# Kernel tuning notes

Hardware: AMD Instinct MI355X
Metric: run time of the kernel (lower is better)

The kernel has to match this reference:

```python
import jax, jax.numpy as jnp
import numpy as np

MODES = (16, 16)
EMBED_DIM = 64
NUM_HEADS = 8


def spectral_conv(x, w):
    """FNO-style spectral conv. x: [B,S,Ci,H,W]; w: [Ci,Co,mx,my,2] (real/imag)."""
    wc = w[..., 0] + 1j * w[..., 1]
    H, W = x.shape[-2], x.shape[-1]
    mx, my = wc.shape[2], wc.shape[3]
    xf = jnp.fft.rfft2(x)                                   # [B,S,Ci,H,W//2+1]
    of = jnp.einsum('bsixy,ioxy->bsoxy', xf[..., :mx, :my], wc)
    out_f = jnp.zeros(x.shape[:2] + (wc.shape[1], H, W // 2 + 1), dtype=of.dtype)
    out_f = out_f.at[..., :mx, :my].set(of)
    return jnp.fft.irfft2(out_f, s=(H, W))


def log_cpb_bias(n_sub_x, n_sub_y, w1, b1, w2):
    """Swin-v2-style log-spaced continuous position bias -> [heads, S, S]."""
    cx = jnp.arange(n_sub_x, dtype=jnp.float32)
    cy = jnp.arange(n_sub_y, dtype=jnp.float32)
    coords = jnp.stack(jnp.meshgrid(cx, cy, indexing='ij'), axis=-1).reshape(-1, 2)
    rel = coords[:, None, :] - coords[None, :, :]           # [S,S,2]
    rel = jnp.sign(rel) * jnp.log1p(jnp.abs(rel))
    h = jax.nn.relu(rel @ w1 + b1)                          # [S,S,hidden]
    bias = h @ w2                                           # [S,S,heads]
    return jnp.transpose(bias, (2, 0, 1))


def _unflatten(f, num_heads, embed_dim):
    # [B,S,h*d,H,W] -> [B,h,S,d,H,W]
    B, S = f.shape[0], f.shape[1]
    f = f.reshape(B, S, num_heads, embed_dim, f.shape[-2], f.shape[-1])
    return jnp.transpose(f, (0, 2, 1, 3, 4, 5))


def setup_inputs() -> dict:
    key = jax.random.key(0)
    ks = jax.random.split(key, 9)
    B, S, D, H, W = 2, 64, EMBED_DIM, 32, 32
    hd = NUM_HEADS * D
    mx, my = MODES
    scale = 0.02
    return {
        'seq': jax.random.normal(ks[0], (B, S, D, H, W), dtype=jnp.float32),
        'wq': scale * jax.random.normal(ks[1], (D, hd, mx, my, 2), dtype=jnp.float32),
        'wk': scale * jax.random.normal(ks[2], (D, hd, mx, my, 2), dtype=jnp.float32),
        'wv': scale * jax.random.normal(ks[3], (D, hd, mx, my, 2), dtype=jnp.float32),
        'wo': scale * jax.random.normal(ks[4], (hd, D, mx, my, 2), dtype=jnp.float32),
        'cpb_w1': scale * jax.random.normal(ks[5], (2, D), dtype=jnp.float32),
        'cpb_b1': jnp.zeros((D,), dtype=jnp.float32),
        'cpb_w2': scale * jax.random.normal(ks[6], (D, NUM_HEADS), dtype=jnp.float32),
        'n_sub_x': 8,
        'n_sub_y': 8,
    }


def reference(seq, wq, wk, wv, wo, cpb_w1, cpb_b1, cpb_w2, n_sub_x, n_sub_y):
    q = _unflatten(spectral_conv(seq, wq), NUM_HEADS, EMBED_DIM)  # [B,h,S,d,H,W]
    k = _unflatten(spectral_conv(seq, wk), NUM_HEADS, EMBED_DIM)
    v = _unflatten(spectral_conv(seq, wv), NUM_HEADS, EMBED_DIM)

    bias = log_cpb_bias(n_sub_x, n_sub_y, cpb_w1, cpb_b1, cpb_w2)  # [h,S,S]

    d, H, W = q.shape[-3], q.shape[-2], q.shape[-1]
    scale = 1.0 / jnp.sqrt(jnp.asarray(d * H * W, dtype=q.dtype))
    scores = jnp.einsum('bhqdxy,bhkdxy->bhqk', q, k) * scale + bias[None]
    attn = jax.nn.softmax(scores, axis=-1)
    sa = jnp.einsum('bhqk,bhkdxy->bhqdxy', attn, v)          # [B,h,S,d,H,W]

    # _flatten: [B,h,S,d,H,W] -> [B,S,h*d,H,W]
    sa = jnp.transpose(sa, (0, 2, 1, 3, 4, 5))
    B, S = sa.shape[0], sa.shape[1]
    sa = sa.reshape(B, S, NUM_HEADS * EMBED_DIM, H, W)
    return spectral_conv(sa, wo)
```

## Files before the change

### kernel.cpp

```cpp
#include <hip/hip_runtime.h>

#define TWO_PI 6.28318530717958647692f

#define NH 8
#define CH 128
#define NCH 2

#define OFF_XM   0ull
#define OFF_WTA  (OFF_XM + 8388608ull)
#define OFF_WTB  (OFF_WTA + 16777216ull)
#define OFF_PO   (OFF_WTB + 16777216ull)
#define OFF_ATTN (OFF_PO + 16777216ull)
#define WS_TOTAL (OFF_ATTN + 262144ull)

typedef short bf16x8 __attribute__((ext_vector_type(8)));
typedef float f32x4 __attribute__((ext_vector_type(4)));
#define MFMA_B16(a, b, c) __builtin_amdgcn_mfma_f32_16x16x32_bf16(a, b, c, 0, 0, 0)

__device__ __forceinline__ float bl(unsigned u) { return __uint_as_float(u << 16); }
__device__ __forceinline__ unsigned short f2b(float f) {
    unsigned u = __float_as_uint(f);
    return (unsigned short)((u + 0x7fffu + ((u >> 16) & 1u)) >> 16);
}
__device__ __forceinline__ unsigned pack2(float lo, float hi) {
    return (unsigned)f2b(lo) | ((unsigned)f2b(hi) << 16);
}

__device__ __forceinline__ bf16x8 mkfrag(const unsigned* __restrict__ Wt, int co_l, int ri,
                                         int ci0, bool dc) {
    unsigned a0 = Wt[(ci0 + 0) * 64 + (co_l ^ (ci0 + 0))];
    unsigned a1 = Wt[(ci0 + 1) * 64 + (co_l ^ (ci0 + 1))];
    unsigned a2 = Wt[(ci0 + 2) * 64 + (co_l ^ (ci0 + 2))];
    unsigned a3 = Wt[(ci0 + 3) * 64 + (co_l ^ (ci0 + 3))];
    uint4 r;
    if (ri) {
        if (dc) { r.x = 0u; r.y = 0u; r.z = 0u; r.w = 0u; }
        else {
            r.x = (a0 >> 16) | (a0 << 16); r.y = (a1 >> 16) | (a1 << 16);
            r.z = (a2 >> 16) | (a2 << 16); r.w = (a3 >> 16) | (a3 << 16);
        }
    } else {
        r.x = a0 ^ 0x80000000u; r.y = a1 ^ 0x80000000u;
        r.z = a2 ^ 0x80000000u; r.w = a3 ^ 0x80000000u;
    }
    return __builtin_bit_cast(bf16x8, r);
}

__global__ __launch_bounds__(256) void k_transpose2(const float* __restrict__ srcA, unsigned* __restrict__ dstA, int kindA,
                                                    const float* __restrict__ srcB, unsigned* __restrict__ dstB, int kindB,
                                                    int m0) {
    const float* in = (blockIdx.z == 0) ? srcA : srcB;
    unsigned* outp = (blockIdx.z == 0) ? dstA : dstB;
    int kind = (blockIdx.z == 0) ? kindA : kindB;
    __shared__ unsigned T[16][65];
    int tid = threadIdx.x;
    int r0 = blockIdx.x * 64;
    int ci, h;
    if (kind == 2) { h = r0 >> 12; ci = (r0 >> 6) & 63; }
    else           { ci = r0 >> 9; h = (r0 >> 6) & 7; }
    int ml0 = blockIdx.y * 16;
    int u = (m0 + ml0) >> 4;
    const float2* in2 = (const float2*)in;
    #pragma unroll
    for (int p = 0; p < 4; ++p) {
        int f = tid + p * 256;
        int row = f >> 4, mc = f & 15;
        float fac = (kind == 0) ? (mc > 0 ? 1.41421356f : (u > 0 ? 0.70710678f : 1.f))
                  : (kind == 1) ? (mc > 0 ? 1.f : (u > 0 ? 0.5f : 1.f)) : 1.f;
        float2 v = in2[(size_t)(r0 + row) * 256 + m0 + ml0 + mc];
        T[mc][row] = pack2(v.x * fac, v.y * fac);
    }
    __syncthreads();
    #pragma unroll
    for (int p = 0; p < 4; ++p) {
        int f = tid + p * 256;
        int ml = f >> 6, co = f & 63;
        outp[((size_t)((ml0 + ml) * 8 + h) << 12) + ci * 64 + co] = T[ml][co];
    }
}

__global__ __launch_bounds__(256) void k_rfft_y(const float* __restrict__ seq,
                                                float2* __restrict__ T) {
    __shared__ float c32[32], s32[32];
    __shared__ float fld[32][33];
    int tid = threadIdx.x;
    int bc = blockIdx.x;
    if (tid < 32) { float s, c; __sincosf(TWO_PI * tid / 32.0f, &s, &c); c32[tid] = c; s32[tid] = s; }
    float4 v = ((const float4*)(seq + (size_t)bc * 1024))[tid];
    int x = tid >> 3, y4 = (tid & 7) * 4;
    fld[x][y4] = v.x; fld[x][y4 + 1] = v.y; fld[x][y4 + 2] = v.z; fld[x][y4 + 3] = v.w;
    __syncthreads();
    float2* op = T + (size_t)bc * 512;
    #pragma unroll
    for (int p = 0; p < 2; ++p) {
        int e = tid + p * 256;
        int xx = e >> 4, vv = e & 15;
        float sr = 0.f, si = 0.f;
        #pragma unroll
        for (int y = 0; y < 32; ++y) {
            float f = fld[xx][y];
            int ph = (vv * y) & 31;
            sr = fmaf(f, c32[ph], sr);
            si = fmaf(-f, s32[ph], si);
        }
        float2 t; t.x = sr; t.y = si;
        op[e] = t;
    }
}

__global__ __launch_bounds__(256) void k_rfft_x(const float2* __restrict__ T,
                                                unsigned short* __restrict__ XM) {
    __shared__ float c32[32], s32[32];
    __shared__ float2 t[8][512];
    int tid = threadIdx.x;
    int cig = blockIdx.x;
    int bs = blockIdx.y;
    if (tid < 32) { float s, c; __sincosf(TWO_PI * tid / 32.0f, &s, &c); c32[tid] = c; s32[tid] = s; }
    const float4* src = (const float4*)(T + ((size_t)bs * 64 + cig * 8) * 512);
    #pragma unroll
    for (int p = 0; p < 8; ++p) {
        int idx = tid + p * 256;
        float4 w = src[idx];
        int ch = idx >> 8, r2 = idx & 255;
        float2 t0; t0.x = w.x; t0.y = w.y;
        float2 t1; t1.x = w.z; t1.y = w.w;
        t[ch][r2 * 2] = t0; t[ch][r2 * 2 + 1] = t1;
    }
    __syncthreads();
    int u = tid >> 4, vv = tid & 15;
    unsigned outw[8];
    for (int ch = 0; ch < 8; ++ch) {
        float xr = 0.f, xi = 0.f;
        #pragma unroll
        for (int x = 0; x < 32; ++x) {
            float2 tv = t[ch][x * 16 + vv];
            int ph = (u * x) & 31;
            float c = c32[ph], s = s32[ph];
            xr += tv.x * c + tv.y * s;
            xi += tv.y * c - tv.x * s;
        }
        outw[ch] = pack2(xr, xi);
    }
    uint4* op = (uint4*)(XM + (((size_t)tid * 128 + bs) * 64 + cig * 8) * 2);
    uint4 a, b;
    a.x = outw[0]; a.y = outw[1]; a.z = outw[2]; a.w = outw[3];
    b.x = outw[4]; b.y = outw[5]; b.z = outw[6]; b.w = outw[7];
    op[0] = a; op[1] = b;
}

__global__ __launch_bounds__(512) void k_qks(const unsigned short* __restrict__ XM,
                                             const unsigned* __restrict__ WQ,
                                             const unsigned* __restrict__ WK,
                                             float* __restrict__ part, int mbase) {
    __shared__ __align__(16) unsigned char Xs[16384];
    __shared__ __align__(16) unsigned Wq[4096];
    __shared__ __align__(16) unsigned Wk[4096];
    __shared__ __align__(16) unsigned char Qs[16384];
    __shared__ __align__(16) unsigned char Ks[16384];
    int tid = threadIdx.x;
    int mg = blockIdx.x, h = blockIdx.y, b = blockIdx.z;
    int lane = tid & 63, w = tid >> 6;
    int lr = lane & 15, lg = lane >> 4;
    int wr = w & 1, wc = w >> 1;
    int sxa = (lr & 7) << 4;
    int ri = lr & 1;
    f32x4 zf = {0.f, 0.f, 0.f, 0.f};
    f32x4 sacc[2];
    sacc[0] = zf; sacc[1] = zf;
    for (int mm = 0; mm < 4; ++mm) {
        int ml = mg * 4 + mm;
        int mode = mbase + ml;
        bool dc = (mode == 0);
        __syncthreads();
        {
            const unsigned short* xg = XM + ((size_t)mode * 128 + b * 64) * 128;
            #pragma unroll
            for (int p = 0; p < 2; ++p) {
                int g = tid + p * 512; int row = g >> 4, c16 = g & 15;
                uint4 v = *(const uint4*)(xg + row * 128 + c16 * 8);
                *(uint4*)(Xs + row * 256 + ((c16 * 16) ^ ((row & 7) << 4))) = v;
            }
        }
        {
            const unsigned* tq = WQ + ((size_t)(ml * 8 + h) << 12);
            const unsigned* tk = WK + ((size_t)(ml * 8 + h) << 12);
            #pragma unroll
            for (int p = 0; p < 16; ++p) {
                int idx = tid + p * 512;
                int r = idx & 4095;
                int ci = r >> 6, co = r & 63;
                if (idx < 4096) Wq[ci * 64 + (co ^ ci)] = tq[r];
                else            Wk[ci * 64 + (co ^ ci)] = tk[r];
            }
        }
        __syncthreads();
        {
            f32x4 qa[2][2], ka[2][2];
            #pragma unroll
            for (int m = 0; m < 2; ++m)
                #pragma unroll
                for (int n = 0; n < 2; ++n) { qa[m][n] = zf; ka[m][n] = zf; }
            #pragma unroll
            for (int ks = 0; ks < 4; ++ks) {
                int kb = (ks * 64 + lg * 16) ^ sxa;
                int ci0 = ks * 16 + lg * 4;
                bf16x8 a0 = *(const bf16x8*)(Xs + (wr * 32 + lr) * 256 + kb);
                bf16x8 a1 = *(const bf16x8*)(Xs + (wr * 32 + 16 + lr) * 256 + kb);
                #pragma unroll
                for (int n = 0; n < 2; ++n) {
                    int co_l = wc * 16 + n * 8 + (lr >> 1);
                    bf16x8 bq = mkfrag(Wq, co_l, ri, ci0, dc);
                    bf16x8 bk = mkfrag(Wk, co_l, ri, ci0, dc);
                    qa[0][n] = MFMA_B16(a0, bq, qa[0][n]);
                    qa[1][n] = MFMA_B16(a1, bq, qa[1][n]);
                    ka[0][n] = MFMA_B16(a0, bk, ka[0][n]);
                    ka[1][n] = MFMA_B16(a1, bk, ka[1][n]);
                }
            }
            #pragma unroll
            for (int m = 0; m < 2; ++m)
                #pragma unroll
                for (int n = 0; n < 2; ++n) {
                    int colb = (wc * 32 + n * 16 + lr) * 2;
                    #pragma unroll
                    for (int r = 0; r < 4; ++r) {
                        int row = wr * 32 + m * 16 + lg * 4 + r;
                        int swz = (row & 7) << 4;
                        *(unsigned short*)(Qs + row * 256 + (colb ^ swz)) = f2b(qa[m][n][r]);
                        *(unsigned short*)(Ks + row * 256 + (colb ^ swz)) = f2b(ka[m][n][r]);
                    }
                }
        }
        __syncthreads();
        {
            #pragma unroll
            for (int ks = 0; ks < 4; ++ks) {
                int kb = (ks * 64 + lg * 16) ^ sxa;
                bf16x8 a0 = *(const bf16x8*)(Qs + (wr * 32 + lr) * 256 + kb);
                bf16x8 a1 = *(const bf16x8*)(Qs + (wr * 32 + 16 + lr) * 256 + kb);
                bf16x8 b0 = *(const bf16x8*)(Ks + (wc * 16 + lr) * 256 + kb);
                sacc[0] = MFMA_B16(a0, b0, sacc[0]);
                sacc[1] = MFMA_B16(a1, b0, sacc[1]);
            }
        }
    }
    float* pp = part + (((size_t)((mbase >> 2) + mg) * 16 + b * 8 + h) << 12);
    #pragma unroll
    for (int m = 0; m < 2; ++m)
        #pragma unroll
        for (int r = 0; r < 4; ++r)
            pp[(wr * 32 + m * 16 + lg * 4 + r) * 64 + wc * 16 + lr] = sacc[m][r];
}

__global__ void k_softmax(const float* __restrict__ part,
                          const float* __restrict__ w1, const float* __restrict__ b1,
                          const float* __restrict__ w2, unsigned short* __restrict__ attnb) {
    int j = threadIdx.x;
    int i = blockIdx.x;
    int bh = blockIdx.y;
    int h = bh & 7;
    float s = 0.f;
    for (int mg = 0; mg < 64; ++mg)
        s += part[(((size_t)mg * 16 + bh) * 64 + i) * 64 + j];
    float dx = (float)((i >> 3) - (j >> 3));
    float dy = (float)((i & 7) - (j & 7));
    float rx = (dx > 0.f ? 1.f : (dx < 0.f ? -1.f : 0.f)) * log1pf(fabsf(dx));
    float ry = (dy > 0.f ? 1.f : (dy < 0.f ? -1.f : 0.f)) * log1pf(fabsf(dy));
    float bias = 0.f;
    for (int l = 0; l < 64; ++l) {
        float hv = fmaxf(rx * w1[l] + ry * w1[64 + l] + b1[l], 0.f);
        bias = fmaf(hv, w2[l * NH + h], bias);
    }
    s = s * (1.0f / 262144.0f) + bias;
    float m = s;
    for (int o = 32; o >= 1; o >>= 1) m = fmaxf(m, __shfl_xor(m, o));
    float e = expf(s - m);
    float t = e;
    for (int o = 32; o >= 1; o >>= 1) t += __shfl_xor(t, o);
    attnb[((size_t)bh * 64 + i) * 64 + j] = f2b(e / t);
}

__global__ __launch_bounds__(512) void k_savo(const unsigned short* __restrict__ XM,
                                              const unsigned* __restrict__ WV,
                                              const unsigned* __restrict__ WO,
                                              const unsigned short* __restrict__ attnb,
                                              float* __restrict__ outf, int mbase) {
    __shared__ __align__(16) unsigned char Xs[16384];
    __shared__ __align__(16) unsigned Wv[4096];
    __shared__ __align__(16) unsigned Wo[4096];
    __shared__ __align__(16) unsigned char Vt[16384];
    __shared__ __align__(16) unsigned char Ss[16384];
    int tid = threadIdx.x;
    int ml = blockIdx.x, b = blockIdx.y;
    int mode = mbase + ml;
    bool dc = (mode == 0);
    int lane = tid & 63, w = tid >> 6;
    int lr = lane & 15, lg = lane >> 4;
    int wr = w & 1, wc = w >> 1;
    int sxa = (lr & 7) << 4;
    int ri = lr & 1;
    f32x4 zf = {0.f, 0.f, 0.f, 0.f};
    {
        const unsigned short* xg = XM + ((size_t)mode * 128 + b * 64) * 128;
        #pragma unroll
        for (int p = 0; p < 2; ++p) {
            int g = tid + p * 512; int row = g >> 4, c16 = g & 15;
            uint4 v = *(const uint4*)(xg + row * 128 + c16 * 8);
            *(uint4*)(Xs + row * 256 + ((c16 * 16) ^ ((row & 7) << 4))) = v;
        }
    }
    f32x4 oacc[2][2];
    oacc[0][0] = zf; oacc[0][1] = zf; oacc[1][0] = zf; oacc[1][1] = zf;
    for (int h = 0; h < NH; ++h) {
        __syncthreads();
        {
            const unsigned* tv = WV + ((size_t)(ml * 8 + h) << 12);
            const unsigned* to = WO + ((size_t)(ml * 8 + h) << 12);
            #pragma unroll
            for (int p = 0; p < 16; ++p) {
                int idx = tid + p * 512;
                int r = idx & 4095;
                int ci = r >> 6, co = r & 63;
                if (idx < 4096) Wv[ci * 64 + (co ^ ci)] = tv[r];
                else            Wo[ci * 64 + (co ^ ci)] = to[r];
            }
        }
        bf16x8 af[2][2];
        #pragma unroll
        for (int m = 0; m < 2; ++m)
            #pragma unroll
            for (int ks = 0; ks < 2; ++ks) {
                int irow = wr * 32 + m * 16 + lr;
                af[m][ks] = *(const bf16x8*)(attnb + (((size_t)(b * 8 + h) * 64 + irow) * 64 + ks * 32 + lg * 8));
            }
        __syncthreads();
        {
            f32x4 va[2][2];
            va[0][0] = zf; va[0][1] = zf; va[1][0] = zf; va[1][1] = zf;
            #pragma unroll
            for (int ks = 0; ks < 4; ++ks) {
                int kb = (ks * 64 + lg * 16) ^ sxa;
                int ci0 = ks * 16 + lg * 4;
                bf16x8 a0 = *(const bf16x8*)(Xs + (wr * 32 + lr) * 256 + kb);
                bf16x8 a1 = *(const bf16x8*)(Xs + (wr * 32 + 16 + lr) * 256 + kb);
                #pragma unroll
                for (int n = 0; n < 2; ++n) {
                    int co_l = wc * 16 + n * 8 + (lr >> 1);
                    bf16x8 bb = mkfrag(Wv, co_l, ri, ci0, dc);
                    va[0][n] = MFMA_B16(a0, bb, va[0][n]);
                    va[1][n] = MFMA_B16(a1, bb, va[1][n]);
                }
            }
            #pragma unroll
            for (int m = 0; m < 2; ++m)
                #pragma unroll
                for (int n = 0; n < 2; ++n) {
                    int cp = wc * 32 + n * 16 + lr;
                    int j0 = wr * 32 + m * 16 + lg * 4;
                    uint2 t;
                    t.x = pack2(va[m][n][0], va[m][n][1]);
                    t.y = pack2(va[m][n][2], va[m][n][3]);
                    *(uint2*)(Vt + cp * 128 + ((j0 * 2) ^ ((cp & 7) << 4))) = t;
                }
        }
        __syncthreads();
        {
            f32x4 sa_[2][2];
            sa_[0][0] = zf; sa_[0][1] = zf; sa_[1][0] = zf; sa_[1][1] = zf;
            #pragma unroll
            for (int ks = 0; ks < 2; ++ks) {
                #pragma unroll
                for (int n = 0; n < 2; ++n) {
                    int cp = wc * 32 + n * 16 + lr;
                    bf16x8 bb = *(const bf16x8*)(Vt + cp * 128 + ((ks * 64 + lg * 16) ^ ((cp & 7) << 4)));
                    sa_[0][n] = MFMA_B16(af[0][ks], bb, sa_[0][n]);
                    sa_[1][n] = MFMA_B16(af[1][ks], bb, sa_[1][n]);
                }
            }
            #pragma unroll
            for (int m = 0; m < 2; ++m)
                #pragma unroll
                for (int n = 0; n < 2; ++n) {
                    int colb = (wc * 32 + n * 16 + lr) * 2;
                    #pragma unroll
                    for (int r = 0; r < 4; ++r) {
                        int row = wr * 32 + m * 16 + lg * 4 + r;
                        *(unsigned short*)(Ss + row * 256 + (colb ^ ((row & 7) << 4))) = f2b(sa_[m][n][r]);
                    }
                }
        }
        __syncthreads();
        {
            #pragma unroll
            for (int ks = 0; ks < 4; ++ks) {
                int kb = (ks * 64 + lg * 16) ^ sxa;
                int ci0 = ks * 16 + lg * 4;
                bf16x8 a0 = *(const bf16x8*)(Ss + (wr * 32 + lr) * 256 + kb);
                bf16x8 a1 = *(const bf16x8*)(Ss + (wr * 32 + 16 + lr) * 256 + kb);
                #pragma unroll
                for (int n = 0; n < 2; ++n) {
                    int co_l = wc * 16 + n * 8 + (lr >> 1);
                    bf16x8 bb = mkfrag(Wo, co_l, ri, ci0, false);
                    oacc[0][n] = MFMA_B16(a0, bb, oacc[0][n]);
                    oacc[1][n] = MFMA_B16(a1, bb, oacc[1][n]);
                }
            }
        }
    }
    #pragma unroll
    for (int m = 0; m < 2; ++m)
        #pragma unroll
        for (int n = 0; n < 2; ++n)
            #pragma unroll
            for (int r = 0; r < 4; ++r) {
                int i = wr * 32 + m * 16 + lg * 4 + r;
                int c2p = wc * 32 + n * 16 + lr;
                outf[((size_t)mode * 128 + b * 64 + i) * 128 + c2p] = oacc[m][n][r];
            }
}

__global__ __launch_bounds__(256) void k_irfft_v(const float* __restrict__ outf,
                                                 float2* __restrict__ G) {
    __shared__ float c32[32], s32[32];
    __shared__ float2 mf[256][8];
    int tid = threadIdx.x;
    int cg = blockIdx.x;
    int bs = blockIdx.y;
    if (tid < 32) { float s, c; __sincosf(TWO_PI * tid / 32.0f, &s, &c); c32[tid] = c; s32[tid] = s; }
    #pragma unroll
    for (int p = 0; p < 4; ++p) {
        int idx = tid + p * 256;
        int mode = idx >> 2, q = idx & 3;
        float4 v = *(const float4*)(outf + ((size_t)mode * 128 + bs) * 128 + cg * 16 + q * 4);
        float2 t0; t0.x = v.x; t0.y = v.y;
        float2 t1; t1.x = v.z; t1.y = v.w;
        mf[mode][q * 2] = t0; mf[mode][q * 2 + 1] = t1;
    }
    __syncthreads();
    #pragma unroll 1
    for (int p = 0; p < 2; ++p) {
        int e = tid + p * 256;
        int u = e >> 5, y = e & 31;
        #pragma unroll 1
        for (int ch = 0; ch < 8; ++ch) {
            float2 f0 = mf[u * 16][ch];
            float fr0 = f0.x;
            float fi0 = (u == 0) ? 0.f : f0.y;
            float ssr = 0.5f * fr0, ssi = 0.5f * fi0;
            #pragma unroll
            for (int v = 1; v < 16; ++v) {
                float2 f = mf[u * 16 + v][ch];
                int ph = (v * y) & 31;
                float c = c32[ph], s = s32[ph];
                ssr += f.x * c - f.y * s;
                ssi += f.x * s + f.y * c;
            }
            float2 g; g.x = ssr; g.y = ssi;
            G[(((size_t)u * 128 + bs) * 64 + cg * 8 + ch) * 32 + y] = g;
        }
    }
}

__global__ __launch_bounds__(256) void k_irfft_u(const float2* __restrict__ G,
                                                 float* __restrict__ out) {
    __shared__ float c32[32], s32[32];
    __shared__ float2 Gs[16][8][32];
    int tid = threadIdx.x;
    int cg = blockIdx.x;
    int bs = blockIdx.y;
    if (tid < 32) { float s, c; __sincosf(TWO_PI * tid / 32.0f, &s, &c); c32[tid] = c; s32[tid] = s; }
    #pragma unroll
    for (int p = 0; p < 8; ++p) {
        int idx = tid + p * 256;
        int y2 = idx & 15, ch = (idx >> 4) & 7, u = idx >> 7;
        float4 v = *(const float4*)((const float*)G + ((((size_t)u * 128 + bs) * 64 + cg * 8 + ch) * 32 + y2 * 2) * 2);
        float2 t0; t0.x = v.x; t0.y = v.y;
        float2 t1; t1.x = v.z; t1.y = v.w;
        Gs[u][ch][y2 * 2] = t0; Gs[u][ch][y2 * 2 + 1] = t1;
    }
    __syncthreads();
    #pragma unroll 1
    for (int p = 0; p < 4; ++p) {
        int pos = tid + p * 256;
        int x = pos >> 5, y = pos & 31;
        #pragma unroll 1
        for (int ch = 0; ch < 8; ++ch) {
            float acc = 0.f;
            #pragma unroll
            for (int u = 0; u < 16; ++u) {
                float2 g = Gs[u][ch][y];
                int ph = (u * x) & 31;
                acc += g.x * c32[ph] - g.y * s32[ph];
            }
            out[((size_t)(bs * 64 + cg * 8 + ch)) * 1024 + x * 32 + y] = acc * (1.0f / 512.0f);
        }
    }
}

extern "C" void kernel_launch(void* const* d_in, const int* in_sizes, int n_in,
                              void* d_out, int out_size, void* d_ws, size_t ws_size,
                              hipStream_t stream) {
    (void)in_sizes; (void)n_in; (void)out_size;
    const float* seq = (const float*)d_in[0];
    const float* wq = (const float*)d_in[1];
    const float* wk = (const float*)d_in[2];
    const float* wv = (const float*)d_in[3];
    const float* wo = (const float*)d_in[4];
    const float* cw1 = (const float*)d_in[5];
    const float* cb1 = (const float*)d_in[6];
    const float* cw2 = (const float*)d_in[7];
    float* out = (float*)d_out;
    char* ws = (char*)d_ws;
    if (ws_size < WS_TOTAL) return;

    unsigned short* XM = (unsigned short*)(ws + OFF_XM);
    unsigned* WTA = (unsigned*)(ws + OFF_WTA);
    unsigned* WTB = (unsigned*)(ws + OFF_WTB);
    float2* Tbuf = (float2*)(ws + OFF_WTA);
    float2* G = (float2*)(ws + OFF_WTA);
    float* PART = (float*)(ws + OFF_PO);
    float* OUTF = (float*)(ws + OFF_PO);
    unsigned short* ATTNB = (unsigned short*)(ws + OFF_ATTN);

    k_rfft_y<<<dim3(8192), dim3(256), 0, stream>>>(seq, Tbuf);
    k_rfft_x<<<dim3(8, 128), dim3(256), 0, stream>>>(Tbuf, XM);

    for (int c = 0; c < NCH; ++c) {
        int m0 = c * CH;
        k_transpose2<<<dim3(512, CH / 16, 2), dim3(256), 0, stream>>>(wq, WTA, 0, wk, WTB, 0, m0);
        k_qks<<<dim3(CH / 4, NH, 2), dim3(512), 0, stream>>>(XM, WTA, WTB, PART, m0);
    }
    k_softmax<<<dim3(64, 16), dim3(64), 0, stream>>>(PART, cw1, cb1, cw2, ATTNB);

    for (int c = 0; c < NCH; ++c) {
        int m0 = c * CH;
        k_transpose2<<<dim3(512, CH / 16, 2), dim3(256), 0, stream>>>(wv, WTA, 1, wo, WTB, 2, m0);
        k_savo<<<dim3(CH, 2), dim3(512), 0, stream>>>(XM, WTA, WTB, ATTNB, OUTF, m0);
    }
    k_irfft_v<<<dim3(8, 128), dim3(256), 0, stream>>>(OUTF, G);
    k_irfft_u<<<dim3(8, 128), dim3(256), 0, stream>>>(G, out);
}
```

Baseline: 351.8 us.

## Alias Q/K/V/S LDS buffers onto input tiles and widen transpose loads

```diff
diff --git a/kernel.cpp b/kernel.cpp
--- a/kernel.cpp
+++ b/kernel.cpp
@@ -60,15 +60,18 @@
     else           { ci = r0 >> 9; h = (r0 >> 6) & 7; }
     int ml0 = blockIdx.y * 16;
     int u = (m0 + ml0) >> 4;
-    const float2* in2 = (const float2*)in;
-    #pragma unroll
-    for (int p = 0; p < 4; ++p) {
+    const float4* in4 = (const float4*)in;
+    float fac1 = (kind == 0) ? 1.41421356f : 1.f;
+    float facu = (kind == 0) ? (u > 0 ? 0.70710678f : 1.f)
+               : (kind == 1) ? (u > 0 ? 0.5f : 1.f) : 1.f;
+    #pragma unroll
+    for (int p = 0; p < 2; ++p) {
         int f = tid + p * 256;
-        int row = f >> 4, mc = f & 15;
-        float fac = (kind == 0) ? (mc > 0 ? 1.41421356f : (u > 0 ? 0.70710678f : 1.f))
-                  : (kind == 1) ? (mc > 0 ? 1.f : (u > 0 ? 0.5f : 1.f)) : 1.f;
-        float2 v = in2[(size_t)(r0 + row) * 256 + m0 + ml0 + mc];
-        T[mc][row] = pack2(v.x * fac, v.y * fac);
+        int row = f >> 3, mc2 = (f & 7) * 2;
+        float4 v = in4[(size_t)(r0 + row) * 128 + ((m0 + ml0) >> 1) + (f & 7)];
+        float fac0 = (mc2 > 0) ? fac1 : facu;
+        T[mc2][row] = pack2(v.x * fac0, v.y * fac0);
+        T[mc2 + 1][row] = pack2(v.z * fac1, v.w * fac1);
     }
     __syncthreads();
     #pragma unroll
@@ -155,8 +158,8 @@
     __shared__ __align__(16) unsigned char Xs[16384];
     __shared__ __align__(16) unsigned Wq[4096];
     __shared__ __align__(16) unsigned Wk[4096];
-    __shared__ __align__(16) unsigned char Qs[16384];
-    __shared__ __align__(16) unsigned char Ks[16384];
+    unsigned char* Qs = Xs;
+    unsigned char* Ks = (unsigned char*)Wq;
     int tid = threadIdx.x;
     int mg = blockIdx.x, h = blockIdx.y, b = blockIdx.z;
     int lane = tid & 63, w = tid >> 6;
@@ -194,8 +197,8 @@
             }
         }
         __syncthreads();
-        {
-            f32x4 qa[2][2], ka[2][2];
+        f32x4 qa[2][2], ka[2][2];
+        {
             #pragma unroll
             for (int m = 0; m < 2; ++m)
                 #pragma unroll
@@ -217,6 +220,9 @@
                     ka[1][n] = MFMA_B16(a1, bk, ka[1][n]);
                 }
             }
+        }
+        __syncthreads();
+        {
             #pragma unroll
             for (int m = 0; m < 2; ++m)
                 #pragma unroll
@@ -288,8 +294,8 @@
     __shared__ __align__(16) unsigned char Xs[16384];
     __shared__ __align__(16) unsigned Wv[4096];
     __shared__ __align__(16) unsigned Wo[4096];
-    __shared__ __align__(16) unsigned char Vt[16384];
-    __shared__ __align__(16) unsigned char Ss[16384];
+    unsigned char* Vt = (unsigned char*)Wv;
+    unsigned char* Ss = (unsigned char*)Wv;
     int tid = threadIdx.x;
     int ml = blockIdx.x, b = blockIdx.y;
     int mode = mbase + ml;
@@ -334,8 +340,8 @@
                 af[m][ks] = *(const bf16x8*)(attnb + (((size_t)(b * 8 + h) * 64 + irow) * 64 + ks * 32 + lg * 8));
             }
         __syncthreads();
-        {
-            f32x4 va[2][2];
+        f32x4 va[2][2];
+        {
             va[0][0] = zf; va[0][1] = zf; va[1][0] = zf; va[1][1] = zf;
             #pragma unroll
             for (int ks = 0; ks < 4; ++ks) {
@@ -351,6 +357,9 @@
                     va[1][n] = MFMA_B16(a1, bb, va[1][n]);
                 }
             }
+        }
+        __syncthreads();
+        {
             #pragma unroll
             for (int m = 0; m < 2; ++m)
                 #pragma unroll
@@ -364,8 +373,8 @@
                 }
         }
         __syncthreads();
-        {
-            f32x4 sa_[2][2];
+        f32x4 sa_[2][2];
+        {
             sa_[0][0] = zf; sa_[0][1] = zf; sa_[1][0] = zf; sa_[1][1] = zf;
             #pragma unroll
             for (int ks = 0; ks < 2; ++ks) {
@@ -377,6 +386,9 @@
                     sa_[1][n] = MFMA_B16(af[1][ks], bb, sa_[1][n]);
                 }
             }
+        }
+        __syncthreads();
+        {
             #pragma unroll
             for (int m = 0; m < 2; ++m)
                 #pragma unroll
```

Result: faster. 335.8 us (-4.5%).
